# Kernel optimization log

Hardware: AMD Instinct MI355X
Metric: run time of the kernel (lower is better)

Reference implementation:

```python
import jax, jax.numpy as jnp
import numpy as np

N, E, IN_C, HID, OUT_C = 50000, 800000, 128, 32, 32
EPS_BN = 1e-5


def gat_layer(x, src, dst, W, a_src, a_dst, bias, heads, out_c, concat):
    n = x.shape[0]
    h = (x @ W).reshape(n, heads, out_c)                    # [N,H,C]
    al_src = jnp.sum(h * a_src, axis=-1)                    # [N,H]
    al_dst = jnp.sum(h * a_dst, axis=-1)                    # [N,H]
    e = jax.nn.leaky_relu(al_src[src] + al_dst[dst], 0.2)   # [Etot,H]
    # segment softmax over incoming edges of each dst node
    m = jax.ops.segment_max(e, dst, num_segments=n)
    e = jnp.exp(e - jax.lax.stop_gradient(m)[dst])
    s = jax.ops.segment_sum(e, dst, num_segments=n)
    alpha = e / (s[dst] + 1e-16)                            # [Etot,H]
    msg = h[src] * alpha[..., None]                         # [Etot,H,C]
    out = jax.ops.segment_sum(msg, dst, num_segments=n)     # [N,H,C]
    out = out.reshape(n, heads * out_c) if concat else out.mean(axis=1)
    return out + bias


def bn_eval(x, w, b, m, v):
    return (x - m) * (w * jax.lax.rsqrt(v + EPS_BN)) + b


def setup_inputs() -> dict:
    key = jax.random.key(0)
    ks = jax.random.split(key, 12)
    f32 = jnp.float32
    inp = {
        'x': jax.random.normal(ks[0], (N, IN_C), dtype=f32),
        'edge_index': jax.random.randint(ks[1], (2, E), 0, N, dtype=jnp.int64),
        'w1': jax.random.normal(ks[2], (IN_C, 4 * HID), dtype=f32) * 0.1,
        'as1': jax.random.normal(ks[3], (4, HID), dtype=f32) * 0.1,
        'ad1': jax.random.normal(ks[4], (4, HID), dtype=f32) * 0.1,
        'b1': jnp.zeros((4 * HID,), f32),
        'bn1_w': jnp.ones((4 * HID,), f32), 'bn1_b': jnp.zeros((4 * HID,), f32),
        'bn1_m': jnp.zeros((4 * HID,), f32), 'bn1_v': jnp.ones((4 * HID,), f32),
        'w2': jax.random.normal(ks[5], (4 * HID, 4 * HID), dtype=f32) * 0.1,
        'as2': jax.random.normal(ks[6], (4, HID), dtype=f32) * 0.1,
        'ad2': jax.random.normal(ks[7], (4, HID), dtype=f32) * 0.1,
        'b2': jnp.zeros((4 * HID,), f32),
        'bn2_w': jnp.ones((4 * HID,), f32), 'bn2_b': jnp.zeros((4 * HID,), f32),
        'bn2_m': jnp.zeros((4 * HID,), f32), 'bn2_v': jnp.ones((4 * HID,), f32),
        'w3': jax.random.normal(ks[8], (4 * HID, OUT_C), dtype=f32) * 0.1,
        'as3': jax.random.normal(ks[9], (1, OUT_C), dtype=f32) * 0.1,
        'ad3': jax.random.normal(ks[10], (1, OUT_C), dtype=f32) * 0.1,
        'b3': jnp.zeros((OUT_C,), f32),
    }
    return inp


def reference(x, edge_index, w1, as1, ad1, b1, bn1_w, bn1_b, bn1_m, bn1_v,
              w2, as2, ad2, b2, bn2_w, bn2_b, bn2_m, bn2_v,
              w3, as3, ad3, b3):
    n = x.shape[0]
    loop = jnp.arange(n, dtype=edge_index.dtype)
    src = jnp.concatenate([edge_index[0], loop])  # add_self_loops (PyG default)
    dst = jnp.concatenate([edge_index[1], loop])
    # layer 1: GAT(heads=4, concat) -> BN(eval) -> relu (dropout=eval identity)
    h = gat_layer(x, src, dst, w1, as1, ad1, b1, 4, HID, True)
    h = jax.nn.relu(bn_eval(h, bn1_w, bn1_b, bn1_m, bn1_v))
    # layer 2
    h = gat_layer(h, src, dst, w2, as2, ad2, b2, 4, HID, True)
    h = jax.nn.relu(bn_eval(h, bn2_w, bn2_b, bn2_m, bn2_v))
    # layer 3: heads=1, concat=False
    return gat_layer(h, src, dst, w3, as3, ad3, b3, 1, OUT_C, False)
```

## Files before the change

### kernel.cpp

```cpp
#include <hip/hip_runtime.h>
#include <hip/hip_fp16.h>
#include <cstdint>


#define NBCHUNK 128
#define MAXBK 512

__device__ __forceinline__ float lrelu02(float x) {
  return x > 0.f ? x : 0.2f * x;
}

__device__ __forceinline__ float expw(float x) {
  return __expf(fminf(x, 80.f));
}

__global__ void detect_kernel(const unsigned* __restrict__ ei, int* __restrict__ flag) {
  int lane = threadIdx.x;
  unsigned w = ei[2 * lane + 1];
  unsigned long long nz = __ballot(w != 0u);
  if (lane == 0) *flag = (nz == 0ull) ? 1 : 0;
}

__global__ __launch_bounds__(256) void bcount_kernel(const void* __restrict__ ei, int E,
                                                     const int* __restrict__ flag,
                                                     int* __restrict__ counts,
                                                     int nbk, int chunk) {
  __shared__ int hist[MAXBK];
  for (int i = threadIdx.x; i < nbk; i += 256) hist[i] = 0;
  __syncthreads();
  int lo = blockIdx.x * chunk;
  int hi = lo + chunk; if (hi > E) hi = E;
  const bool is64 = (*flag) != 0;
  for (int e = lo + threadIdx.x; e < hi; e += 256) {
    int d = is64 ? (int)((const long long*)ei)[(size_t)E + e] : ((const int*)ei)[E + e];
    atomicAdd(&hist[d >> 7], 1);
  }
  __syncthreads();
  for (int i = threadIdx.x; i < nbk; i += 256)
    counts[(size_t)blockIdx.x * nbk + i] = hist[i];
}

__global__ void bscanT_kernel(int* __restrict__ counts, int* __restrict__ T, int nbk) {
  int b = blockIdx.x;
  int t = threadIdx.x;
  int lane = t & 63;
  int v = counts[(size_t)t * nbk + b];
  int inc = v;
#pragma unroll
  for (int off = 1; off < 64; off <<= 1) {
    int u = __shfl_up(inc, off);
    if (lane >= off) inc += u;
  }
  __shared__ int w0;
  if (t == 63) w0 = inc;
  __syncthreads();
  int wb = (t >= 64) ? w0 : 0;
  counts[(size_t)t * nbk + b] = wb + inc - v;
  if (t == 127) T[b] = wb + inc;
}

__global__ void bscanE_kernel(const int* __restrict__ T, int* __restrict__ EB, int nbk) {
  int lane = threadIdx.x;
  int carry = 0;
  for (int start = 0; start < nbk; start += 64) {
    int i = start + lane;
    int v = (i < nbk) ? T[i] : 0;
    int inc = v;
#pragma unroll
    for (int off = 1; off < 64; off <<= 1) {
      int u = __shfl_up(inc, off);
      if (lane >= off) inc += u;
    }
    if (i < nbk) EB[i] = inc - v + carry;
    carry += __shfl(inc, 63);
  }
  if (lane == 0) EB[nbk] = carry;
}

__global__ __launch_bounds__(256) void bemit_kernel(const void* __restrict__ ei, int E,
                                                    const int* __restrict__ flag,
                                                    const int* __restrict__ counts,
                                                    const int* __restrict__ EB,
                                                    int nbk, int chunk,
                                                    unsigned* __restrict__ binned) {
  __shared__ int cur[MAXBK];
  for (int i = threadIdx.x; i < nbk; i += 256)
    cur[i] = counts[(size_t)blockIdx.x * nbk + i] + EB[i];
  __syncthreads();
  int lo = blockIdx.x * chunk;
  int hi = lo + chunk; if (hi > E) hi = E;
  const bool is64 = (*flag) != 0;
  for (int e = lo + threadIdx.x; e < hi; e += 256) {
    int s, d;
    if (is64) {
      const long long* p = (const long long*)ei;
      s = (int)p[e];
      d = (int)p[(size_t)E + e];
    } else {
      const int* p = (const int*)ei;
      s = p[e];
      d = p[E + e];
    }
    int pos = atomicAdd(&cur[d >> 7], 1);
    binned[pos] = ((unsigned)(d & 127) << 16) | (unsigned)s;
  }
}

__global__ __launch_bounds__(256) void bscatter2_kernel(const unsigned* __restrict__ binned,
                                                        const int* __restrict__ EB,
                                                        int* __restrict__ row_ptr,
                                                        int* __restrict__ csr_src,
                                                        int n, int E) {
  __shared__ int hist[128];
  __shared__ int cur[128];
  __shared__ int w0s;
  const int b = blockIdx.x;
  const int t = threadIdx.x;
  const int bb = b << 7;
  if (t < 128) hist[t] = 0;
  __syncthreads();
  const int lo = EB[b], hi = EB[b + 1];
  for (int i = lo + t; i < hi; i += 256)
    atomicAdd(&hist[binned[i] >> 16], 1);
  __syncthreads();
  int lane = t & 63;
  int v = (t < 128) ? hist[t] : 0;
  int inc = v;
#pragma unroll
  for (int off = 1; off < 64; off <<= 1) {
    int u = __shfl_up(inc, off);
    if (lane >= off) inc += u;
  }
  if (t == 63) w0s = inc;
  __syncthreads();
  int exc = ((t >= 64 && t < 128) ? w0s : 0) + inc - v;
  if (t < 128 && bb + t < n) {
    int rp = EB[b] + bb + t + exc;
    row_ptr[bb + t] = rp;
    csr_src[rp] = bb + t;
    cur[t] = rp + 1;
  }
  if (b == 0 && t == 0) row_ptr[n] = E + n;
  __syncthreads();
  for (int i = lo + t; i < hi; i += 256) {
    unsigned pv = binned[i];
    int pos = atomicAdd(&cur[pv >> 16], 1);
    csr_src[pos] = (int)(pv & 0xFFFFu);
  }
}

template <int BROWS, int BCOLS, int TR, int H, typename AT>
__global__ __launch_bounds__(256) void gemm_al_kernel(const AT* __restrict__ A,
                                                      const float* __restrict__ W,
                                                      const float* __restrict__ a_src,
                                                      const float* __restrict__ a_dst,
                                                      __half* __restrict__ Hout,
                                                      float* __restrict__ alS,
                                                      float* __restrict__ alD,
                                                      int n, int OUTC) {
  constexpr int TC = 4;
  constexpr int CG = BCOLS / TC;
  constexpr int RG = BROWS / TR;
  static_assert(CG * RG == 256, "256 threads");
  constexpr int AP = 132;
  constexpr bool A16 = (sizeof(AT) == 2);

  __shared__ __align__(16) float A_lds[BROWS * AP];
  __shared__ __align__(16) float W_lds[128 * BCOLS];

  const int r0 = blockIdx.x * BROWS;
  const int cb = blockIdx.y * BCOLS;
  const int t = threadIdx.x;

  if constexpr (!A16) {
#pragma unroll
    for (int i = 0; i < BROWS / 8; ++i) {
      int slot = t + i * 256;
      int r = slot >> 5;
      int kq = slot & 31;
      float4 v = make_float4(0.f, 0.f, 0.f, 0.f);
      if (r0 + r < n) v = *(const float4*)((const float*)A + (size_t)(r0 + r) * 128 + kq * 4);
      *(float4*)&A_lds[r * AP + kq * 4] = v;
    }
  } else {
#pragma unroll
    for (int i = 0; i < BROWS / 16; ++i) {
      int slot = t + i * 256;
      int r = slot >> 4;
      int q = slot & 15;
      uint4 raw = make_uint4(0u, 0u, 0u, 0u);
      if (r0 + r < n) raw = *(const uint4*)((const __half*)A + (size_t)(r0 + r) * 128 + q * 8);
      const __half2* hp = (const __half2*)&raw;
      float2 f0 = __half22float2(hp[0]);
      float2 f1 = __half22float2(hp[1]);
      float2 f2 = __half22float2(hp[2]);
      float2 f3 = __half22float2(hp[3]);
      *(float4*)&A_lds[r * AP + q * 8] = make_float4(f0.x, f0.y, f1.x, f1.y);
      *(float4*)&A_lds[r * AP + q * 8 + 4] = make_float4(f2.x, f2.y, f3.x, f3.y);
    }
  }
#pragma unroll
  for (int i = 0; i < BCOLS / 8; ++i) {
    int slot = t + i * 256;
    int k = slot / (BCOLS / 4);
    int cq = slot % (BCOLS / 4);
    float4 v = *(const float4*)(W + (size_t)k * OUTC + cb + cq * 4);
    *(float4*)&W_lds[k * BCOLS + cq * 4] = v;
  }
  __syncthreads();

  const int cg = t % CG;
  const int rg = t / CG;

  float acc[TR][TC];
#pragma unroll
  for (int i = 0; i < TR; ++i)
#pragma unroll
    for (int j = 0; j < TC; ++j) acc[i][j] = 0.f;

  for (int k4 = 0; k4 < 32; ++k4) {
    float av[TR][4];
#pragma unroll
    for (int i = 0; i < TR; ++i) {
      float4 a4 = *(const float4*)&A_lds[(rg * TR + i) * AP + k4 * 4];
      av[i][0] = a4.x; av[i][1] = a4.y; av[i][2] = a4.z; av[i][3] = a4.w;
    }
#pragma unroll
    for (int kk = 0; kk < 4; ++kk) {
      float4 w4 = *(const float4*)&W_lds[(k4 * 4 + kk) * BCOLS + cg * TC];
#pragma unroll
      for (int i = 0; i < TR; ++i) {
        acc[i][0] = fmaf(av[i][kk], w4.x, acc[i][0]);
        acc[i][1] = fmaf(av[i][kk], w4.y, acc[i][1]);
        acc[i][2] = fmaf(av[i][kk], w4.z, acc[i][2]);
        acc[i][3] = fmaf(av[i][kk], w4.w, acc[i][3]);
      }
    }
  }

#pragma unroll
  for (int i = 0; i < TR; ++i) {
    int r = r0 + rg * TR + i;
    if (r >= n) continue;
    __half2 lo = __floats2half2_rn(acc[i][0], acc[i][1]);
    __half2 hi = __floats2half2_rn(acc[i][2], acc[i][3]);
    uint2 pk;
    pk.x = *(const unsigned*)&lo;
    pk.y = *(const unsigned*)&hi;
    *(uint2*)(Hout + (size_t)r * OUTC + cb + cg * TC) = pk;
  }

  const int head = (cb + cg * TC) >> 5;
  const int cLoc = (cg & 7) * 4;
  float as_c[4], ad_c[4];
#pragma unroll
  for (int j = 0; j < 4; ++j) {
    as_c[j] = a_src[head * 32 + cLoc + j];
    ad_c[j] = a_dst[head * 32 + cLoc + j];
  }
#pragma unroll
  for (int i = 0; i < TR; ++i) {
    float ps = acc[i][0] * as_c[0] + acc[i][1] * as_c[1] +
               acc[i][2] * as_c[2] + acc[i][3] * as_c[3];
    float pd = acc[i][0] * ad_c[0] + acc[i][1] * ad_c[1] +
               acc[i][2] * ad_c[2] + acc[i][3] * ad_c[3];
#pragma unroll
    for (int off = 1; off < 8; off <<= 1) {
      ps += __shfl_xor(ps, off);
      pd += __shfl_xor(pd, off);
    }
    if ((cg & 7) == 0) {
      int r = r0 + rg * TR + i;
      if (r < n) {
        alS[(size_t)r * H + head] = ps;
        alD[(size_t)r * H + head] = pd;
      }
    }
  }
}

template <int H, bool BN, typename OutT>
__global__ __launch_bounds__(256) void agg_kernel(
    const int* __restrict__ row_ptr, const int* __restrict__ csr_src,
    const float* __restrict__ alS, const float* __restrict__ alD,
    const __half* __restrict__ hfeat, const float* __restrict__ bias,
    const float* __restrict__ bnw, const float* __restrict__ bnb,
    const float* __restrict__ bnm, const float* __restrict__ bnv,
    OutT* __restrict__ out, int n) {
  constexpr int LPN = (H == 4) ? 64 : 32;
  constexpr int NPB = 256 / LPN;
  constexpr int KCAP = 96;
  constexpr int RSH = (H == 4) ? 8 : 6;

  __shared__ __align__(16) float sW[NPB][KCAP * H];
  __shared__ int sOff[NPB][KCAP];

  const int slot = threadIdx.x / LPN;
  const int sl = threadIdx.x % LPN;
  const int v = blockIdx.x * NPB + slot;
  const bool active = v < n;
  const char* hb = (const char*)hfeat;

  int rs = 0, re = 0;
  if (active) { rs = row_ptr[v]; re = row_ptr[v + 1]; }
  const int deg = re - rs;
  const int degS = deg < KCAP ? deg : KCAP;

  if constexpr (H == 4) {
    float4 ad4 = make_float4(0.f, 0.f, 0.f, 0.f);
    if (active) ad4 = *(const float4*)(alD + (size_t)v * 4);
    float den0 = 0.f, den1 = 0.f, den2 = 0.f, den3 = 0.f;
    for (int k = sl; k < degS; k += 64) {
      int s = csr_src[rs + k];
      sOff[slot][k] = s << RSH;
      float4 a4 = *(const float4*)(alS + (size_t)s * 4);
      float u0 = expw(lrelu02(a4.x + ad4.x));
      float u1 = expw(lrelu02(a4.y + ad4.y));
      float u2 = expw(lrelu02(a4.z + ad4.z));
      float u3 = expw(lrelu02(a4.w + ad4.w));
      ((float4*)&sW[slot][0])[k] = make_float4(u0, u1, u2, u3);
      den0 += u0; den1 += u1; den2 += u2; den3 += u3;
    }
#pragma unroll
    for (int off = 32; off >= 1; off >>= 1) {
      den0 += __shfl_xor(den0, off);
      den1 += __shfl_xor(den1, off);
      den2 += __shfl_xor(den2, off);
      den3 += __shfl_xor(den3, off);
    }

    const int c = 2 * sl;
    const int h = sl >> 4;
    const unsigned cb2 = (unsigned)(c * 2);
    float2 acc = make_float2(0.f, 0.f);
    int j = 0;
    for (; j + 4 <= degS; j += 4) {
      unsigned o0 = (unsigned)sOff[slot][j + 0] + cb2;
      unsigned o1 = (unsigned)sOff[slot][j + 1] + cb2;
      unsigned o2 = (unsigned)sOff[slot][j + 2] + cb2;
      unsigned o3 = (unsigned)sOff[slot][j + 3] + cb2;
      float w0 = sW[slot][(j + 0) * 4 + h];
      float w1 = sW[slot][(j + 1) * 4 + h];
      float w2 = sW[slot][(j + 2) * 4 + h];
      float w3 = sW[slot][(j + 3) * 4 + h];
      float2 f0 = __half22float2(*(const __half2*)(hb + o0));
      float2 f1 = __half22float2(*(const __half2*)(hb + o1));
      float2 f2 = __half22float2(*(const __half2*)(hb + o2));
      float2 f3 = __half22float2(*(const __half2*)(hb + o3));
      acc.x = fmaf(w0, f0.x, acc.x); acc.y = fmaf(w0, f0.y, acc.y);
      acc.x = fmaf(w1, f1.x, acc.x); acc.y = fmaf(w1, f1.y, acc.y);
      acc.x = fmaf(w2, f2.x, acc.x); acc.y = fmaf(w2, f2.y, acc.y);
      acc.x = fmaf(w3, f3.x, acc.x); acc.y = fmaf(w3, f3.y, acc.y);
    }
    for (; j < degS; ++j) {
      unsigned o = (unsigned)sOff[slot][j] + cb2;
      float w = sW[slot][j * 4 + h];
      float2 f = __half22float2(*(const __half2*)(hb + o));
      acc.x = fmaf(w, f.x, acc.x); acc.y = fmaf(w, f.y, acc.y);
    }
    float den = (h == 0) ? den0 : (h == 1) ? den1 : (h == 2) ? den2 : den3;
    if (deg > KCAP) {
      float adh = alD[(size_t)v * 4 + h];
      for (int e = rs + KCAP; e < re; ++e) {
        int s = csr_src[e];
        float u = expw(lrelu02(alS[(size_t)s * 4 + h] + adh));
        den += u;
        float2 f = __half22float2(*(const __half2*)(hb + ((unsigned)(s << RSH) + cb2)));
        acc.x = fmaf(u, f.x, acc.x); acc.y = fmaf(u, f.y, acc.y);
      }
    }
    if (active) {
      float inv = 1.f / (den + 1e-16f);
      float2 b2v = *(const float2*)(bias + c);
      float g0 = acc.x * inv + b2v.x;
      float g1 = acc.y * inv + b2v.y;
      if constexpr (BN) {
        float2 bw = *(const float2*)(bnw + c);
        float2 bb = *(const float2*)(bnb + c);
        float2 bm = *(const float2*)(bnm + c);
        float2 bv = *(const float2*)(bnv + c);
        g0 = (g0 - bm.x) * (bw.x * rsqrtf(bv.x + 1e-5f)) + bb.x;
        g1 = (g1 - bm.y) * (bw.y * rsqrtf(bv.y + 1e-5f)) + bb.y;
        g0 = fmaxf(g0, 0.f);
        g1 = fmaxf(g1, 0.f);
      }
      if constexpr (sizeof(OutT) == 2) {
        __half2 o2 = __floats2half2_rn(g0, g1);
        *(__half2*)((__half*)out + (size_t)v * 128 + c) = o2;
      } else {
        *(float2*)((float*)out + (size_t)v * 128 + c) = make_float2(g0, g1);
      }
    }
  } else {
    float ad = active ? alD[v] : 0.f;
    float den = 0.f;
    for (int k = sl; k < degS; k += 32) {
      int s = csr_src[rs + k];
      sOff[slot][k] = s << RSH;
      float u = expw(lrelu02(alS[s] + ad));
      sW[slot][k] = u;
      den += u;
    }
#pragma unroll
    for (int off = 16; off >= 1; off >>= 1) den += __shfl_xor(den, off);

    const int c = sl;
    const unsigned cb2 = (unsigned)(c * 2);
    float acc = 0.f;
    int j = 0;
    for (; j + 4 <= degS; j += 4) {
      unsigned o0 = (unsigned)sOff[slot][j + 0] + cb2;
      unsigned o1 = (unsigned)sOff[slot][j + 1] + cb2;
      unsigned o2 = (unsigned)sOff[slot][j + 2] + cb2;
      unsigned o3 = (unsigned)sOff[slot][j + 3] + cb2;
      float w0 = sW[slot][j + 0], w1 = sW[slot][j + 1];
      float w2 = sW[slot][j + 2], w3 = sW[slot][j + 3];
      float f0 = __half2float(*(const __half*)(hb + o0));
      float f1 = __half2float(*(const __half*)(hb + o1));
      float f2 = __half2float(*(const __half*)(hb + o2));
      float f3 = __half2float(*(const __half*)(hb + o3));
      acc = fmaf(w0, f0, acc); acc = fmaf(w1, f1, acc);
      acc = fmaf(w2, f2, acc); acc = fmaf(w3, f3, acc);
    }
    for (; j < degS; ++j) {
      unsigned o = (unsigned)sOff[slot][j] + cb2;
      float w = sW[slot][j];
      acc = fmaf(w, __half2float(*(const __half*)(hb + o)), acc);
    }
    if (deg > KCAP) {
      for (int e = rs + KCAP; e < re; ++e) {
        int s = csr_src[e];
        float u = expw(lrelu02(alS[s] + ad));
        den += u;
        acc = fmaf(u, __half2float(*(const __half*)(hb + ((unsigned)(s << RSH) + cb2))), acc);
      }
    }
    if (active) {
      ((float*)out)[(size_t)v * 32 + c] = acc / (den + 1e-16f) + bias[c];
    }
  }
}

extern "C" void kernel_launch(void* const* d_in, const int* in_sizes, int n_in,
                              void* d_out, int out_size, void* d_ws, size_t ws_size,
                              hipStream_t stream) {
  const float* x = (const float*)d_in[0];
  const void* ei = d_in[1];
  const float* w1 = (const float*)d_in[2];
  const float* as1 = (const float*)d_in[3];
  const float* ad1 = (const float*)d_in[4];
  const float* b1 = (const float*)d_in[5];
  const float* bn1w = (const float*)d_in[6];
  const float* bn1b = (const float*)d_in[7];
  const float* bn1m = (const float*)d_in[8];
  const float* bn1v = (const float*)d_in[9];
  const float* w2 = (const float*)d_in[10];
  const float* as2 = (const float*)d_in[11];
  const float* ad2 = (const float*)d_in[12];
  const float* b2 = (const float*)d_in[13];
  const float* bn2w = (const float*)d_in[14];
  const float* bn2b = (const float*)d_in[15];
  const float* bn2m = (const float*)d_in[16];
  const float* bn2v = (const float*)d_in[17];
  const float* w3 = (const float*)d_in[18];
  const float* as3 = (const float*)d_in[19];
  const float* ad3 = (const float*)d_in[20];
  const float* b3 = (const float*)d_in[21];

  const int N = in_sizes[0] / 128;
  const int E = in_sizes[1] / 2;
  const int nbk = (N + 127) / 128;
  const int chunk = (E + NBCHUNK - 1) / NBCHUNK;

  char* base = (char*)d_ws;
  size_t off = 0;
  auto alloc = [&](size_t bytes) {
    void* p = base + off;
    off = (off + bytes + 255) & ~(size_t)255;
    return p;
  };
  int* flag = (int*)alloc(4);
  int* counts = (int*)alloc((size_t)NBCHUNK * nbk * 4);
  int* T = (int*)alloc((size_t)nbk * 4);
  int* EB = (int*)alloc((size_t)(nbk + 1) * 4);
  unsigned* binned = (unsigned*)alloc((size_t)E * 4);
  int* row_ptr = (int*)alloc((size_t)(N + 1) * 4);
  int* csr_src = (int*)alloc((size_t)(E + N) * 4);
  __half* hbuf = (__half*)alloc((size_t)N * 128 * 2);
  __half* gbuf = (__half*)alloc((size_t)N * 128 * 2);
  float* alS = (float*)alloc((size_t)N * 4 * 4);
  float* alD = (float*)alloc((size_t)N * 4 * 4);
  (void)ws_size;

  detect_kernel<<<1, 64, 0, stream>>>((const unsigned*)ei, flag);
  bcount_kernel<<<NBCHUNK, 256, 0, stream>>>(ei, E, flag, counts, nbk, chunk);
  bscanT_kernel<<<nbk, NBCHUNK, 0, stream>>>(counts, T, nbk);
  bscanE_kernel<<<1, 64, 0, stream>>>(T, EB, nbk);
  bemit_kernel<<<NBCHUNK, 256, 0, stream>>>(ei, E, flag, counts, EB, nbk, chunk, binned);
  bscatter2_kernel<<<nbk, 256, 0, stream>>>(binned, EB, row_ptr, csr_src, N, E);

  const int rowBlocks = (N + 63) / 64;

  gemm_al_kernel<64, 64, 4, 4, float><<<dim3(rowBlocks, 2), 256, 0, stream>>>(
      x, w1, as1, ad1, hbuf, alS, alD, N, 128);
  agg_kernel<4, true, __half><<<(N + 3) / 4, 256, 0, stream>>>(
      row_ptr, csr_src, alS, alD, hbuf, b1, bn1w, bn1b, bn1m, bn1v, gbuf, N);
  gemm_al_kernel<64, 64, 4, 4, __half><<<dim3(rowBlocks, 2), 256, 0, stream>>>(
      gbuf, w2, as2, ad2, hbuf, alS, alD, N, 128);
  agg_kernel<4, true, __half><<<(N + 3) / 4, 256, 0, stream>>>(
      row_ptr, csr_src, alS, alD, hbuf, b2, bn2w, bn2b, bn2m, bn2v, gbuf, N);
  gemm_al_kernel<64, 32, 2, 1, __half><<<dim3(rowBlocks, 1), 256, 0, stream>>>(
      gbuf, w3, as3, ad3, hbuf, alS, alD, N, 32);
  agg_kernel<1, false, float><<<(N + 7) / 8, 256, 0, stream>>>(
      row_ptr, csr_src, alS, alD, hbuf, b3, nullptr, nullptr, nullptr, nullptr,
      (float*)d_out, N);
}
```

Measured before the change: 222.6 us.

## Replace scalar FP32 GEMM with MFMA f16 GEMM and pre-transposed f16 weights

The three dense projection GEMMs move from a scalar FMA tiling to the 16x16x32 f16 MFMA instruction. Each block now covers the full output width, and the A tile is staged in LDS as half precision. A small kernel converts each weight matrix to f16 in transposed layout before every GEMM. The change cuts GEMM compute time and LDS footprint, at the cost of three extra launches, f16 rounding of x and the weights, and scalar half stores for the output.

New measurement: 199.2 us. -10.5%, faster.

```diff
diff --git a/kernel.cpp b/kernel.cpp
--- a/kernel.cpp
+++ b/kernel.cpp
@@ -5,6 +5,9 @@
 
 #define NBCHUNK 128
 #define MAXBK 512
+
+typedef _Float16 f16x8 __attribute__((ext_vector_type(8)));
+typedef float f32x4 __attribute__((ext_vector_type(4)));
 
 __device__ __forceinline__ float lrelu02(float x) {
   return x > 0.f ? x : 0.2f * x;
@@ -149,131 +152,110 @@
   }
 }
 
-template <int BROWS, int BCOLS, int TR, int H, typename AT>
-__global__ __launch_bounds__(256) void gemm_al_kernel(const AT* __restrict__ A,
-                                                      const float* __restrict__ W,
-                                                      const float* __restrict__ a_src,
-                                                      const float* __restrict__ a_dst,
-                                                      __half* __restrict__ Hout,
-                                                      float* __restrict__ alS,
-                                                      float* __restrict__ alD,
-                                                      int n, int OUTC) {
-  constexpr int TC = 4;
-  constexpr int CG = BCOLS / TC;
-  constexpr int RG = BROWS / TR;
-  static_assert(CG * RG == 256, "256 threads");
-  constexpr int AP = 132;
-  constexpr bool A16 = (sizeof(AT) == 2);
-
-  __shared__ __align__(16) float A_lds[BROWS * AP];
-  __shared__ __align__(16) float W_lds[128 * BCOLS];
-
-  const int r0 = blockIdx.x * BROWS;
-  const int cb = blockIdx.y * BCOLS;
+__global__ void wcvt_kernel(const float* __restrict__ W, _Float16* __restrict__ Wt,
+                            int OUTC) {
+  int idx = blockIdx.x * 256 + threadIdx.x;
+  if (idx >= 128 * OUTC) return;
+  int k = idx / OUTC, c = idx % OUTC;
+  Wt[(size_t)c * 128 + k] = (_Float16)W[idx];
+}
+
+template <int OUTC, int H, typename AT>
+__global__ __launch_bounds__(256) void mfma_gemm_al_kernel(
+    const AT* __restrict__ A, const _Float16* __restrict__ Wt,
+    const float* __restrict__ a_src, const float* __restrict__ a_dst,
+    __half* __restrict__ Hout, float* __restrict__ alS, float* __restrict__ alD,
+    int n) {
+  constexpr int NT = OUTC / 16;
+  constexpr int APH = 136;
+
+  __shared__ __align__(16) _Float16 A_lds[64 * APH];
+  __shared__ __align__(16) _Float16 W_lds[OUTC * APH];
+
   const int t = threadIdx.x;
-
-  if constexpr (!A16) {
-#pragma unroll
-    for (int i = 0; i < BROWS / 8; ++i) {
+  const int r0 = blockIdx.x * 64;
+
+  if constexpr (sizeof(AT) == 4) {
+#pragma unroll
+    for (int i = 0; i < 8; ++i) {
       int slot = t + i * 256;
-      int r = slot >> 5;
-      int kq = slot & 31;
+      int r = slot >> 5, q = slot & 31;
       float4 v = make_float4(0.f, 0.f, 0.f, 0.f);
-      if (r0 + r < n) v = *(const float4*)((const float*)A + (size_t)(r0 + r) * 128 + kq * 4);
-      *(float4*)&A_lds[r * AP + kq * 4] = v;
+      if (r0 + r < n) v = *(const float4*)((const float*)A + (size_t)(r0 + r) * 128 + q * 4);
+      __half2 p0 = __floats2half2_rn(v.x, v.y);
+      __half2 p1 = __floats2half2_rn(v.z, v.w);
+      uint2 pk;
+      pk.x = *(unsigned*)&p0;
+      pk.y = *(unsigned*)&p1;
+      *(uint2*)&A_lds[r * APH + q * 4] = pk;
     }
   } else {
 #pragma unroll
-    for (int i = 0; i < BROWS / 16; ++i) {
+    for (int i = 0; i < 4; ++i) {
       int slot = t + i * 256;
-      int r = slot >> 4;
-      int q = slot & 15;
+      int r = slot >> 4, q = slot & 15;
       uint4 raw = make_uint4(0u, 0u, 0u, 0u);
       if (r0 + r < n) raw = *(const uint4*)((const __half*)A + (size_t)(r0 + r) * 128 + q * 8);
-      const __half2* hp = (const __half2*)&raw;
-      float2 f0 = __half22float2(hp[0]);
-      float2 f1 = __half22float2(hp[1]);
-      float2 f2 = __half22float2(hp[2]);
-      float2 f3 = __half22float2(hp[3]);
-      *(float4*)&A_lds[r * AP + q * 8] = make_float4(f0.x, f0.y, f1.x, f1.y);
-      *(float4*)&A_lds[r * AP + q * 8 + 4] = make_float4(f2.x, f2.y, f3.x, f3.y);
-    }
-  }
-#pragma unroll
-  for (int i = 0; i < BCOLS / 8; ++i) {
+      *(uint4*)&A_lds[r * APH + q * 8] = raw;
+    }
+  }
+#pragma unroll
+  for (int i = 0; i < OUTC / 16; ++i) {
     int slot = t + i * 256;
-    int k = slot / (BCOLS / 4);
-    int cq = slot % (BCOLS / 4);
-    float4 v = *(const float4*)(W + (size_t)k * OUTC + cb + cq * 4);
-    *(float4*)&W_lds[k * BCOLS + cq * 4] = v;
-  }
-  __syncthreads();
-
-  const int cg = t % CG;
-  const int rg = t / CG;
-
-  float acc[TR][TC];
-#pragma unroll
-  for (int i = 0; i < TR; ++i)
-#pragma unroll
-    for (int j = 0; j < TC; ++j) acc[i][j] = 0.f;
-
-  for (int k4 = 0; k4 < 32; ++k4) {
-    float av[TR][4];
-#pragma unroll
-    for (int i = 0; i < TR; ++i) {
-      float4 a4 = *(const float4*)&A_lds[(rg * TR + i) * AP + k4 * 4];
-      av[i][0] = a4.x; av[i][1] = a4.y; av[i][2] = a4.z; av[i][3] = a4.w;
-    }
-#pragma unroll
-    for (int kk = 0; kk < 4; ++kk) {
-      float4 w4 = *(const float4*)&W_lds[(k4 * 4 + kk) * BCOLS + cg * TC];
-#pragma unroll
-      for (int i = 0; i < TR; ++i) {
-        acc[i][0] = fmaf(av[i][kk], w4.x, acc[i][0]);
-        acc[i][1] = fmaf(av[i][kk], w4.y, acc[i][1]);
-        acc[i][2] = fmaf(av[i][kk], w4.z, acc[i][2]);
-        acc[i][3] = fmaf(av[i][kk], w4.w, acc[i][3]);
+    int c = slot >> 4, q = slot & 15;
+    uint4 raw = *(const uint4*)(Wt + (size_t)c * 128 + q * 8);
+    *(uint4*)&W_lds[c * APH + q * 8] = raw;
+  }
+  __syncthreads();
+
+  const int w = t >> 6;
+  const int lane = t & 63;
+  const int lrow = lane & 15;
+  const int lk = lane >> 4;
+
+  f32x4 acc[NT];
+#pragma unroll
+  for (int i = 0; i < NT; ++i) acc[i] = (f32x4){0.f, 0.f, 0.f, 0.f};
+
+#pragma unroll
+  for (int kc = 0; kc < 4; ++kc) {
+    f16x8 a = *(const f16x8*)&A_lds[(w * 16 + lrow) * APH + kc * 32 + lk * 8];
+#pragma unroll
+    for (int ct = 0; ct < NT; ++ct) {
+      f16x8 b = *(const f16x8*)&W_lds[(ct * 16 + lrow) * APH + kc * 32 + lk * 8];
+      acc[ct] = __builtin_amdgcn_mfma_f32_16x16x32_f16(a, b, acc[ct], 0, 0, 0);
+    }
+  }
+
+  const int rbase = r0 + w * 16 + lk * 4;
+#pragma unroll
+  for (int ct = 0; ct < NT; ++ct) {
+#pragma unroll
+    for (int j = 0; j < 4; ++j) {
+      int r = rbase + j;
+      if (r < n) Hout[(size_t)r * OUTC + ct * 16 + lrow] = __float2half(acc[ct][j]);
+    }
+  }
+
+#pragma unroll
+  for (int h = 0; h < H; ++h) {
+    float as0 = a_src[h * 32 + lrow], as1 = a_src[h * 32 + 16 + lrow];
+    float ad0 = a_dst[h * 32 + lrow], ad1 = a_dst[h * 32 + 16 + lrow];
+#pragma unroll
+    for (int j = 0; j < 4; ++j) {
+      float ps = acc[2 * h][j] * as0 + acc[2 * h + 1][j] * as1;
+      float pd = acc[2 * h][j] * ad0 + acc[2 * h + 1][j] * ad1;
+#pragma unroll
+      for (int off = 1; off < 16; off <<= 1) {
+        ps += __shfl_xor(ps, off);
+        pd += __shfl_xor(pd, off);
       }
-    }
-  }
-
-#pragma unroll
-  for (int i = 0; i < TR; ++i) {
-    int r = r0 + rg * TR + i;
-    if (r >= n) continue;
-    __half2 lo = __floats2half2_rn(acc[i][0], acc[i][1]);
-    __half2 hi = __floats2half2_rn(acc[i][2], acc[i][3]);
-    uint2 pk;
-    pk.x = *(const unsigned*)&lo;
-    pk.y = *(const unsigned*)&hi;
-    *(uint2*)(Hout + (size_t)r * OUTC + cb + cg * TC) = pk;
-  }
-
-  const int head = (cb + cg * TC) >> 5;
-  const int cLoc = (cg & 7) * 4;
-  float as_c[4], ad_c[4];
-#pragma unroll
-  for (int j = 0; j < 4; ++j) {
-    as_c[j] = a_src[head * 32 + cLoc + j];
-    ad_c[j] = a_dst[head * 32 + cLoc + j];
-  }
-#pragma unroll
-  for (int i = 0; i < TR; ++i) {
-    float ps = acc[i][0] * as_c[0] + acc[i][1] * as_c[1] +
-               acc[i][2] * as_c[2] + acc[i][3] * as_c[3];
-    float pd = acc[i][0] * ad_c[0] + acc[i][1] * ad_c[1] +
-               acc[i][2] * ad_c[2] + acc[i][3] * ad_c[3];
-#pragma unroll
-    for (int off = 1; off < 8; off <<= 1) {
-      ps += __shfl_xor(ps, off);
-      pd += __shfl_xor(pd, off);
-    }
-    if ((cg & 7) == 0) {
-      int r = r0 + rg * TR + i;
-      if (r < n) {
-        alS[(size_t)r * H + head] = ps;
-        alD[(size_t)r * H + head] = pd;
+      if (lrow == 0) {
+        int r = rbase + j;
+        if (r < n) {
+          alS[(size_t)r * H + h] = ps;
+          alD[(size_t)r * H + h] = pd;
+        }
       }
     }
   }
@@ -486,6 +468,7 @@
   unsigned* binned = (unsigned*)alloc((size_t)E * 4);
   int* row_ptr = (int*)alloc((size_t)(N + 1) * 4);
   int* csr_src = (int*)alloc((size_t)(E + N) * 4);
+  _Float16* Wt16 = (_Float16*)alloc((size_t)128 * 128 * 2);
   __half* hbuf = (__half*)alloc((size_t)N * 128 * 2);
   __half* gbuf = (__half*)alloc((size_t)N * 128 * 2);
   float* alS = (float*)alloc((size_t)N * 4 * 4);
@@ -501,16 +484,19 @@
 
   const int rowBlocks = (N + 63) / 64;
 
-  gemm_al_kernel<64, 64, 4, 4, float><<<dim3(rowBlocks, 2), 256, 0, stream>>>(
-      x, w1, as1, ad1, hbuf, alS, alD, N, 128);
+  wcvt_kernel<<<(128 * 128 + 255) / 256, 256, 0, stream>>>(w1, Wt16, 128);
+  mfma_gemm_al_kernel<128, 4, float><<<rowBlocks, 256, 0, stream>>>(
+      x, Wt16, as1, ad1, hbuf, alS, alD, N);
   agg_kernel<4, true, __half><<<(N + 3) / 4, 256, 0, stream>>>(
       row_ptr, csr_src, alS, alD, hbuf, b1, bn1w, bn1b, bn1m, bn1v, gbuf, N);
-  gemm_al_kernel<64, 64, 4, 4, __half><<<dim3(rowBlocks, 2), 256, 0, stream>>>(
-      gbuf, w2, as2, ad2, hbuf, alS, alD, N, 128);
+  wcvt_kernel<<<(128 * 128 + 255) / 256, 256, 0, stream>>>(w2, Wt16, 128);
+  mfma_gemm_al_kernel<128, 4, __half><<<rowBlocks, 256, 0, stream>>>(
+      gbuf, Wt16, as2, ad2, hbuf, alS, alD, N);
   agg_kernel<4, true, __half><<<(N + 3) / 4, 256, 0, stream>>>(
       row_ptr, csr_src, alS, alD, hbuf, b2, bn2w, bn2b, bn2m, bn2v, gbuf, N);
-  gemm_al_kernel<64, 32, 2, 1, __half><<<dim3(rowBlocks, 1), 256, 0, stream>>>(
-      gbuf, w3, as3, ad3, hbuf, alS, alD, N, 32);
+  wcvt_kernel<<<(128 * 32 + 255) / 256, 256, 0, stream>>>(w3, Wt16, 32);
+  mfma_gemm_al_kernel<32, 1, __half><<<rowBlocks, 256, 0, stream>>>(
+      gbuf, Wt16, as3, ad3, hbuf, alS, alD, N);
   agg_kernel<1, false, float><<<(N + 7) / 8, 256, 0, stream>>>(
       row_ptr, csr_src, alS, alD, hbuf, b3, nullptr, nullptr, nullptr, nullptr,
       (float*)d_out, N);
```
